# Kernel optimization log

Hardware: AMD Instinct MI355X
Metric: run time of the kernel (lower is better)

## Reference

```python
import jax, jax.numpy as jnp
import numpy as np
from jax import lax

GRID_SIZE = 5
SPLINE_ORDER = 3
N_COEF = GRID_SIZE + SPLINE_ORDER  # 8 b-spline basis functions per input
GRID_LO, GRID_HI = -1.0, 1.0


def _grid():
    h = (GRID_HI - GRID_LO) / GRID_SIZE
    return jnp.arange(-SPLINE_ORDER, GRID_SIZE + SPLINE_ORDER + 1, dtype=jnp.float32) * h + GRID_LO


def _bsplines(x):
    # x: [..., in] -> [..., in, N_COEF] via Cox-de Boor recursion (efficient-kan)
    grid = _grid()
    x = x[..., None]
    bases = ((x >= grid[:-1]) & (x < grid[1:])).astype(x.dtype)
    for j in range(1, SPLINE_ORDER + 1):
        bases = ((x - grid[:-(j + 1)]) / (grid[j:-1] - grid[:-(j + 1)]) * bases[..., :-1]
                 + (grid[j + 1:] - x) / (grid[j + 1:] - grid[1:-j]) * bases[..., 1:])
    return bases


def _kan_linear(x, base_w, spline_w):
    # x: [..., in]; base_w: [out, in]; spline_w: [out, in, N_COEF]
    base = jax.nn.silu(x) @ base_w.T
    b = _bsplines(x).reshape(x.shape[:-1] + (-1,))  # [..., in*N_COEF]
    return base + b @ spline_w.reshape(spline_w.shape[0], -1).T


def _kan_conv(x, base_w, spline_w):
    # x: [B, C, H, W]; 3x3 valid KAN convolution
    patches = lax.conv_general_dilated_patches(x, (3, 3), (1, 1), 'VALID')  # [B, C*9, H-2, W-2]
    p = patches.transpose(0, 2, 3, 1)  # [B, Ho, Wo, C*9]
    out = _kan_linear(p, base_w, spline_w)  # [B, Ho, Wo, out]
    return out.transpose(0, 3, 1, 2)


def _maxpool2(x):
    return lax.reduce_window(x, -jnp.inf, lax.max, (1, 1, 2, 2), (1, 1, 2, 2), 'VALID')


def setup_inputs() -> dict:
    key = jax.random.key(0)
    ks = jax.random.split(key, 12)
    B = 2048
    x = jax.random.uniform(ks[0], (B, 1, 28, 28), dtype=jnp.float32)
    s = 0.1
    return {
        'x': x,
        'bw1': jax.random.normal(ks[1], (5, 9), dtype=jnp.float32) * s,
        'sw1': jax.random.normal(ks[2], (5, 9, N_COEF), dtype=jnp.float32) * s,
        'bw2': jax.random.normal(ks[3], (5, 45), dtype=jnp.float32) * s,
        'sw2': jax.random.normal(ks[4], (5, 45, N_COEF), dtype=jnp.float32) * s,
        'bw3': jax.random.normal(ks[5], (2, 45), dtype=jnp.float32) * s,
        'sw3': jax.random.normal(ks[6], (2, 45, N_COEF), dtype=jnp.float32) * s,
        'w1': jax.random.normal(ks[7], (500, 162), dtype=jnp.float32) * 0.05,
        'b1': jnp.zeros((500,), dtype=jnp.float32),
        'w2': jax.random.normal(ks[8], (10, 500), dtype=jnp.float32) * 0.05,
        'b2': jnp.zeros((10,), dtype=jnp.float32),
    }


def reference(x, bw1, sw1, bw2, sw2, bw3, sw3, w1, b1, w2, b2):
    h = _kan_conv(x, bw1, sw1)       # [B, 5, 26, 26]
    h = _maxpool2(h)                 # [B, 5, 13, 13]
    h = _kan_conv(h, bw2, sw2)       # [B, 5, 11, 11]
    h = _kan_conv(h, bw3, sw3)       # [B, 2, 9, 9]
    h = h.reshape(h.shape[0], -1)    # [B, 162]
    h = jax.nn.relu(h @ w1.T + b1)   # [B, 500]
    return h @ w2.T + b2             # [B, 10]
```

## Files before the change

kernel.cpp:

```cpp
#include <hip/hip_runtime.h>


typedef _Float16 h2 __attribute__((ext_vector_type(2)));

__device__ __forceinline__ h2 u2h(unsigned int u) {
  union { unsigned int x; h2 h; } v; v.x = u; return v.h;
}
__device__ __forceinline__ unsigned short f2h_bits(float x) {
  union { _Float16 h; unsigned short u; } v; v.h = (_Float16)x; return v.u;
}
__device__ __forceinline__ float h2f(unsigned short u) {
  union { unsigned short u; _Float16 h; } v; v.u = u; return (float)v.h;
}
__device__ __forceinline__ unsigned int pack2h(float a, float b) {
  return (unsigned int)f2h_bits(a) | ((unsigned int)f2h_bits(b) << 16);
}
__device__ __forceinline__ float fdot2(h2 a, h2 b, float c) {
  return __builtin_amdgcn_fdot2(a, b, c, false);
}

__device__ __forceinline__ void featurize_regs(float v, uint4& bs, float& silu) {
  silu = v / (1.0f + __expf(-v));
  bs.x = 0u; bs.y = 0u; bs.z = 0u; bs.w = 0u;
  float u = fmaf(v, 2.5f, 5.5f);
  if (u >= 0.0f && u < 11.0f) {
    float tf = floorf(u);
    float f = u - tf, f2 = f * f, f3 = f2 * f, om = 1.0f - f;
    const float c6 = 1.0f / 6.0f;
    float w0 = om * om * om * c6;
    float w1 = (3.0f * f3 - 6.0f * f2 + 4.0f) * c6;
    float w2 = (-3.0f * f3 + 3.0f * f2 + 3.0f * f + 1.0f) * c6;
    float w3 = f3 * c6;
    unsigned long long w01 =
        (unsigned long long)f2h_bits(w0) |
        ((unsigned long long)f2h_bits(w1) << 16) |
        ((unsigned long long)f2h_bits(w2) << 32) |
        ((unsigned long long)f2h_bits(w3) << 48);
    int t = (int)tf;
    int s = 16 * t - 48;
    unsigned long long lo, hi;
    if (s >= 0) {
      lo = (s < 64) ? (w01 << s) : 0ull;
      hi = (s == 0) ? 0ull : ((s < 64) ? (w01 >> (64 - s)) : (w01 << (s - 64)));
    } else {
      lo = w01 >> (-s);
      hi = 0ull;
    }
    bs.x = (unsigned int)lo; bs.y = (unsigned int)(lo >> 32);
    bs.z = (unsigned int)hi; bs.w = (unsigned int)(hi >> 32);
  }
}

template <int NO, int CHS, int ROWW>
__device__ __forceinline__ void kconv_plain(
    const uint4* bas, const unsigned short* slu,
    const uint4* __restrict__ wS, const float* __restrict__ wB,
    int y0, int x0, float (&acc)[NO]) {
  const uint4* wp = wS;
  const float* bp = wB;
  int baC = y0 * ROWW + x0;
  #pragma unroll 1
  for (int c = 0; c < 5; ++c) {
    int ba = baC;
    #pragma unroll 1
    for (int ky = 0; ky < 3; ++ky) {
      uint4 q0 = bas[ba], q1 = bas[ba + 1], q2 = bas[ba + 2];
      float s0 = h2f(slu[ba]), s1 = h2f(slu[ba + 1]), s2 = h2f(slu[ba + 2]);
      #pragma unroll
      for (int kx = 0; kx < 3; ++kx) {
        uint4 q = (kx == 0) ? q0 : ((kx == 1) ? q1 : q2);
        float sl = (kx == 0) ? s0 : ((kx == 1) ? s1 : s2);
        h2 a0 = u2h(q.x), a1 = u2h(q.y), a2 = u2h(q.z), a3 = u2h(q.w);
        #pragma unroll
        for (int j = 0; j < NO; ++j) {
          uint4 w = wp[kx * NO + j];
          float a = acc[j];
          a = fdot2(a0, u2h(w.x), a);
          a = fdot2(a1, u2h(w.y), a);
          a = fdot2(a2, u2h(w.z), a);
          a = fdot2(a3, u2h(w.w), a);
          acc[j] = fmaf(sl, bp[kx * NO + j], a);
        }
      }
      wp += 3 * NO; bp += 3 * NO;
      ba += ROWW;
    }
    baC += CHS;
  }
}

__global__ __launch_bounds__(256) void k_prep(
    const float* __restrict__ bw1, const float* __restrict__ sw1,
    const float* __restrict__ bw2, const float* __restrict__ sw2,
    const float* __restrict__ bw3, const float* __restrict__ sw3,
    const float* __restrict__ w1, const float* __restrict__ w2,
    unsigned int* __restrict__ V1s, float* __restrict__ V1b,
    unsigned int* __restrict__ V2G0s, float* __restrict__ V2G0b,
    unsigned int* __restrict__ V2G1s, float* __restrict__ V2G1b,
    unsigned int* __restrict__ V3Gs, float* __restrict__ V3Gb,
    unsigned int* __restrict__ W1p4, float* __restrict__ W2p) {
  int t = blockIdx.x * 256 + threadIdx.x;
  if (t < 180) {
    int p = t & 3, o = (t >> 2) % 5, in = t / 20;
    V1s[t] = pack2h(sw1[(o * 9 + in) * 8 + 2 * p], sw1[(o * 9 + in) * 8 + 2 * p + 1]);
  }
  if (t < 45)  { int o = t % 5, in = t / 5; V1b[t] = bw1[o * 9 + in]; }
  if (t < 540) {
    int p = t & 3, u4 = t >> 2;
    int j = u4 % 3, kx = (u4 / 3) % 3, cky = u4 / 9;
    int in = (cky / 3) * 9 + (cky % 3) * 3 + kx;
    V2G0s[t] = pack2h(sw2[(j * 45 + in) * 8 + 2 * p], sw2[(j * 45 + in) * 8 + 2 * p + 1]);
  }
  if (t < 135) {
    int j = t % 3, kx = (t / 3) % 3, cky = t / 9;
    int in = (cky / 3) * 9 + (cky % 3) * 3 + kx;
    V2G0b[t] = bw2[j * 45 + in];
  }
  if (t < 360) {
    int p = t & 3, u4 = t >> 2;
    int j = u4 % 2, kx = (u4 / 2) % 3, cky = u4 / 6;
    int o = 3 + j;
    int in = (cky / 3) * 9 + (cky % 3) * 3 + kx;
    V2G1s[t] = pack2h(sw2[(o * 45 + in) * 8 + 2 * p], sw2[(o * 45 + in) * 8 + 2 * p + 1]);
  }
  if (t < 90) {
    int j = t % 2, kx = (t / 2) % 3, cky = t / 6;
    int o = 3 + j;
    int in = (cky / 3) * 9 + (cky % 3) * 3 + kx;
    V2G1b[t] = bw2[o * 45 + in];
  }
  if (t < 360) {
    int p = t & 3, u4 = t >> 2;
    int kx = u4 % 3, cky = (u4 / 3) % 15, ou = u4 / 45;
    int in = (cky / 3) * 9 + (cky % 3) * 3 + kx;
    V3Gs[t] = pack2h(sw3[(ou * 45 + in) * 8 + 2 * p], sw3[(ou * 45 + in) * 8 + 2 * p + 1]);
  }
  if (t < 90) {
    int kx = t % 3, cky = (t / 3) % 15, ou = t / 45;
    int in = (cky / 3) * 9 + (cky % 3) * 3 + kx;
    V3Gb[t] = bw3[ou * 45 + in];
  }
  if (t < 43008) {
    int j = t & 3, o = (t >> 2) & 511, g = t >> 11;
    int kp = g * 4 + j;
    W1p4[t] = (o < 500 && kp < 81)
                  ? pack2h(w1[o * 162 + 2 * kp], w1[o * 162 + 2 * kp + 1])
                  : 0u;
  }
  if (t < 5120) {
    int o = t >> 9, k = t & 511;
    W2p[t] = (k < 500) ? w2[o * 500 + k] : 0.0f;
  }
}

__global__ __launch_bounds__(256, 8) void k_fused(
    const float* __restrict__ x,
    const unsigned int* __restrict__ V1s, const float* __restrict__ V1b,
    const unsigned int* __restrict__ V2G0s, const float* __restrict__ V2G0b,
    const unsigned int* __restrict__ V2G1s, const float* __restrict__ V2G1b,
    const unsigned int* __restrict__ V3Gs, const float* __restrict__ V3Gb,
    const unsigned int* __restrict__ W1p4, const float* __restrict__ W2p,
    const float* __restrict__ b1, const float* __restrict__ b2,
    float* __restrict__ out) {
  __shared__ uint4 bas[845];
  __shared__ unsigned short slu16[848];
  __shared__ float red[40];
  float*        basF = (float*)bas;
  float*        h3f  = basF + 2048;
  unsigned int* hpk  = (unsigned int*)basF + 2560;
  const int b = blockIdx.x;
  const int tid = threadIdx.x;

  #pragma unroll 1
  for (int l = tid; l < 784; l += 256) {
    uint4 bs; float sl;
    featurize_regs(x[b * 784 + l], bs, sl);
    bas[l] = bs; slu16[l] = f2h_bits(sl);
  }
  __syncthreads();

  float h1v[5];
  if (tid < 169) {
    int py = tid / 13, px = tid % 13;
    int rowbase = (py * 2) * 28 + px * 2;
    float wacc[4][5];
    #pragma unroll
    for (int wi = 0; wi < 4; ++wi)
      #pragma unroll
      for (int o = 0; o < 5; ++o) wacc[wi][o] = 0.0f;
    const unsigned int* wp = V1s;
    const float* bp = V1b;
    int ba = rowbase;
    #pragma unroll 1
    for (int ky = 0; ky < 3; ++ky) {
      #pragma unroll 1
      for (int kx = 0; kx < 3; ++kx) {
        uint4 q00 = bas[ba],      q01 = bas[ba + 1];
        uint4 q10 = bas[ba + 28], q11 = bas[ba + 29];
        float s00 = h2f(slu16[ba]),      s01 = h2f(slu16[ba + 1]);
        float s10 = h2f(slu16[ba + 28]), s11 = h2f(slu16[ba + 29]);
        #pragma unroll
        for (int dy = 0; dy < 2; ++dy) {
          #pragma unroll
          for (int dx = 0; dx < 2; ++dx) {
            uint4 q  = dy ? (dx ? q11 : q10) : (dx ? q01 : q00);
            float sl = dy ? (dx ? s11 : s10) : (dx ? s01 : s00);
            h2 a0 = u2h(q.x), a1 = u2h(q.y), a2 = u2h(q.z), a3 = u2h(q.w);
            #pragma unroll
            for (int o = 0; o < 5; ++o) {
              float a = wacc[dy * 2 + dx][o];
              a = fdot2(a0, u2h(wp[o * 4 + 0]), a);
              a = fdot2(a1, u2h(wp[o * 4 + 1]), a);
              a = fdot2(a2, u2h(wp[o * 4 + 2]), a);
              a = fdot2(a3, u2h(wp[o * 4 + 3]), a);
              wacc[dy * 2 + dx][o] = fmaf(sl, bp[o], a);
            }
          }
        }
        wp += 20; bp += 5;
        ba += 1;
      }
      ba += 25;
    }
    #pragma unroll
    for (int o = 0; o < 5; ++o)
      h1v[o] = fmaxf(fmaxf(wacc[0][o], wacc[1][o]),
                     fmaxf(wacc[2][o], wacc[3][o]));
  }
  __syncthreads();
  if (tid < 169) {
    #pragma unroll
    for (int o = 0; o < 5; ++o) {
      uint4 bs; float sl;
      featurize_regs(h1v[o], bs, sl);
      bas[o * 169 + tid] = bs; slu16[o * 169 + tid] = f2h_bits(sl);
    }
  }
  __syncthreads();

  int og = __builtin_amdgcn_readfirstlane(tid >> 7);
  int p2 = tid & 127;
  float acc2a[3] = {0.0f, 0.0f, 0.0f};
  float acc2b[2] = {0.0f, 0.0f};
  {
    int pc = (p2 < 121) ? p2 : 120;
    int y0 = pc / 11, x0 = pc % 11;
    if (og == 0)
      kconv_plain<3, 169, 13>(bas, slu16, (const uint4*)V2G0s, V2G0b, y0, x0, acc2a);
    else
      kconv_plain<2, 169, 13>(bas, slu16, (const uint4*)V2G1s, V2G1b, y0, x0, acc2b);
  }
  __syncthreads();
  if (p2 < 121) {
    if (og == 0) {
      #pragma unroll
      for (int j = 0; j < 3; ++j) {
        uint4 bs; float sl;
        featurize_regs(acc2a[j], bs, sl);
        bas[j * 121 + p2] = bs; slu16[j * 121 + p2] = f2h_bits(sl);
      }
    } else {
      #pragma unroll
      for (int j = 0; j < 2; ++j) {
        uint4 bs; float sl;
        featurize_regs(acc2b[j], bs, sl);
        bas[(3 + j) * 121 + p2] = bs; slu16[(3 + j) * 121 + p2] = f2h_bits(sl);
      }
    }
  }
  __syncthreads();

  float acc3[1] = {0.0f};
  {
    int pc = (p2 < 81) ? p2 : 80;
    int y0 = pc / 9, x0 = pc % 9;
    kconv_plain<1, 121, 11>(bas, slu16, (const uint4*)V3Gs + og * 45,
                            V3Gb + og * 45, y0, x0, acc3);
  }
  __syncthreads();
  if (p2 < 81) h3f[og * 81 + p2] = acc3[0];
  __syncthreads();
  if (tid < 84)
    hpk[tid] = (tid < 81) ? pack2h(h3f[2 * tid], h3f[2 * tid + 1]) : 0u;
  __syncthreads();

  float fa[2] = {0.0f, 0.0f};
  {
    const uint4* hp4 = (const uint4*)hpk;
    const uint4* wbase = (const uint4*)W1p4 + tid;
    uint4 wA[2], wB[2];
    #pragma unroll
    for (int i = 0; i < 2; ++i) wA[i] = wbase[i * 256];
    #pragma unroll 1
    for (int g = 0; g < 21; g += 2) {
      if (g + 1 < 21) {
        const uint4* p = wbase + (g + 1) * 512;
        #pragma unroll
        for (int i = 0; i < 2; ++i) wB[i] = p[i * 256];
      }
      {
        uint4 hk = hp4[g];
        #pragma unroll
        for (int i = 0; i < 2; ++i) {
          float a = fa[i];
          a = fdot2(u2h(hk.x), u2h(wA[i].x), a);
          a = fdot2(u2h(hk.y), u2h(wA[i].y), a);
          a = fdot2(u2h(hk.z), u2h(wA[i].z), a);
          a = fdot2(u2h(hk.w), u2h(wA[i].w), a);
          fa[i] = a;
        }
      }
      if (g + 2 < 21) {
        const uint4* p = wbase + (g + 2) * 512;
        #pragma unroll
        for (int i = 0; i < 2; ++i) wA[i] = p[i * 256];
      }
      if (g + 1 < 21) {
        uint4 hk = hp4[g + 1];
        #pragma unroll
        for (int i = 0; i < 2; ++i) {
          float a = fa[i];
          a = fdot2(u2h(hk.x), u2h(wB[i].x), a);
          a = fdot2(u2h(hk.y), u2h(wB[i].y), a);
          a = fdot2(u2h(hk.z), u2h(wB[i].z), a);
          a = fdot2(u2h(hk.w), u2h(wB[i].w), a);
          fa[i] = a;
        }
      }
    }
  }
  #pragma unroll
  for (int i = 0; i < 2; ++i) {
    int o = tid + 256 * i;
    float bb = (o < 500) ? b1[o] : 0.0f;
    float v = fa[i] + bb;
    basF[o] = (v > 0.0f && o < 500) ? v : 0.0f;
  }
  __syncthreads();

  float acc10[10];
  {
    float2 ha = ((const float2*)basF)[tid];
    #pragma unroll
    for (int o = 0; o < 10; ++o) {
      float2 w = ((const float2*)&W2p[o * 512])[tid];
      acc10[o] = ha.x * w.x + ha.y * w.y;
    }
  }
  #pragma unroll
  for (int off = 32; off > 0; off >>= 1) {
    #pragma unroll
    for (int o = 0; o < 10; ++o) acc10[o] += __shfl_down(acc10[o], off);
  }
  if ((tid & 63) == 0) {
    int wid = tid >> 6;
    #pragma unroll
    for (int o = 0; o < 10; ++o) red[wid * 10 + o] = acc10[o];
  }
  __syncthreads();
  if (tid < 10)
    out[b * 10 + tid] = red[tid] + red[10 + tid] + red[20 + tid] + red[30 + tid] + b2[tid];
}

extern "C" void kernel_launch(void* const* d_in, const int* in_sizes, int n_in,
                              void* d_out, int out_size, void* d_ws, size_t ws_size,
                              hipStream_t stream) {
  (void)in_sizes; (void)n_in; (void)out_size; (void)ws_size;
  const float* x   = (const float*)d_in[0];
  const float* bw1 = (const float*)d_in[1];
  const float* sw1 = (const float*)d_in[2];
  const float* bw2 = (const float*)d_in[3];
  const float* sw2 = (const float*)d_in[4];
  const float* bw3 = (const float*)d_in[5];
  const float* sw3 = (const float*)d_in[6];
  const float* w1  = (const float*)d_in[7];
  const float* b1  = (const float*)d_in[8];
  const float* w2  = (const float*)d_in[9];
  const float* b2  = (const float*)d_in[10];
  float* out = (float*)d_out;

  char* ws = (char*)d_ws;
  unsigned int* V1s   = (unsigned int*)(ws);
  float*        V1b   = (float*)(ws + 768);
  unsigned int* V2G0s = (unsigned int*)(ws + 1024);
  unsigned int* V2G1s = (unsigned int*)(ws + 3200);
  unsigned int* V3Gs  = (unsigned int*)(ws + 4640);
  float*        V2G0b = (float*)(ws + 6080);
  float*        V2G1b = (float*)(ws + 6624);
  float*        V3Gb  = (float*)(ws + 6984);
  float*        W2p   = (float*)(ws + 7680);
  unsigned int* W1p4  = (unsigned int*)(ws + 28672);

  k_prep<<<168, 256, 0, stream>>>(bw1, sw1, bw2, sw2, bw3, sw3, w1, w2,
                                  V1s, V1b, V2G0s, V2G0b, V2G1s, V2G1b,
                                  V3Gs, V3Gb, W1p4, W2p);
  k_fused<<<2048, 256, 0, stream>>>(x, V1s, V1b, V2G0s, V2G0b, V2G1s, V2G1b,
                                    V3Gs, V3Gb, W1p4, W2p, b1, b2, out);
}
```

Measured before the change: 128.2 us.

## Move KAN conv layers 1 and 2 onto MFMA 16x16x32 f16 matrix ops

```diff
diff --git a/kernel.cpp b/kernel.cpp
--- a/kernel.cpp
+++ b/kernel.cpp
@@ -2,6 +2,10 @@
 
 
 typedef _Float16 h2 __attribute__((ext_vector_type(2)));
+typedef _Float16 f16x8 __attribute__((ext_vector_type(8)));
+typedef float f32x4 __attribute__((ext_vector_type(4)));
+
+union U4H { uint4 u; f16x8 h; };
 
 __device__ __forceinline__ h2 u2h(unsigned int u) {
   union { unsigned int x; h2 h; } v; v.x = u; return v.h;
@@ -17,6 +21,13 @@
 }
 __device__ __forceinline__ float fdot2(h2 a, h2 b, float c) {
   return __builtin_amdgcn_fdot2(a, b, c, false);
+}
+
+__device__ __forceinline__ constexpr int off1(int t) {
+  return (t / 3) * 28 + (t % 3);
+}
+__device__ __forceinline__ constexpr int off2v(int t) {
+  return (t / 9) * 169 + ((t % 9) / 3) * 13 + ((t % 9) % 3);
 }
 
 __device__ __forceinline__ void featurize_regs(float v, uint4& bs, float& silu) {
@@ -94,40 +105,43 @@
     const float* __restrict__ bw2, const float* __restrict__ sw2,
     const float* __restrict__ bw3, const float* __restrict__ sw3,
     const float* __restrict__ w1, const float* __restrict__ w2,
-    unsigned int* __restrict__ V1s, float* __restrict__ V1b,
-    unsigned int* __restrict__ V2G0s, float* __restrict__ V2G0b,
-    unsigned int* __restrict__ V2G1s, float* __restrict__ V2G1b,
+    unsigned int* __restrict__ Bc1g, unsigned int* __restrict__ B2g,
     unsigned int* __restrict__ V3Gs, float* __restrict__ V3Gb,
     unsigned int* __restrict__ W1p4, float* __restrict__ W2p) {
   int t = blockIdx.x * 256 + threadIdx.x;
-  if (t < 180) {
-    int p = t & 3, o = (t >> 2) % 5, in = t / 20;
-    V1s[t] = pack2h(sw1[(o * 9 + in) * 8 + 2 * p], sw1[(o * 9 + in) * 8 + 2 * p + 1]);
-  }
-  if (t < 45)  { int o = t % 5, in = t / 5; V1b[t] = bw1[o * 9 + in]; }
-  if (t < 540) {
-    int p = t & 3, u4 = t >> 2;
-    int j = u4 % 3, kx = (u4 / 3) % 3, cky = u4 / 9;
-    int in = (cky / 3) * 9 + (cky % 3) * 3 + kx;
-    V2G0s[t] = pack2h(sw2[(j * 45 + in) * 8 + 2 * p], sw2[(j * 45 + in) * 8 + 2 * p + 1]);
-  }
-  if (t < 135) {
-    int j = t % 3, kx = (t / 3) % 3, cky = t / 9;
-    int in = (cky / 3) * 9 + (cky % 3) * 3 + kx;
-    V2G0b[t] = bw2[j * 45 + in];
-  }
-  if (t < 360) {
-    int p = t & 3, u4 = t >> 2;
-    int j = u4 % 2, kx = (u4 / 2) % 3, cky = u4 / 6;
-    int o = 3 + j;
-    int in = (cky / 3) * 9 + (cky % 3) * 3 + kx;
-    V2G1s[t] = pack2h(sw2[(o * 45 + in) * 8 + 2 * p], sw2[(o * 45 + in) * 8 + 2 * p + 1]);
-  }
-  if (t < 90) {
-    int j = t % 2, kx = (t / 2) % 3, cky = t / 6;
-    int o = 3 + j;
-    int in = (cky / 3) * 9 + (cky % 3) * 3 + kx;
-    V2G1b[t] = bw2[o * 45 + in];
+  if (t < 1280) {
+    int i = t & 3, l = (t >> 2) & 63, s = t >> 8;
+    int k = s * 32 + ((l >> 4) & 3) * 8 + 2 * i;
+    int col = l & 15, tap = k >> 4, slot = k & 15;
+    unsigned int v = 0u;
+    if (col < 5 && tap < 9) {
+      if (slot < 8) {
+        const float* sp = sw1 + (col * 9 + tap) * 8 + slot;
+        v = pack2h(sp[0], sp[1]);
+      } else if (slot == 8) {
+        float bv = bw1[col * 9 + tap];
+        float hi = (float)(_Float16)bv;
+        v = pack2h(hi, bv - hi);
+      }
+    }
+    Bc1g[t] = v;
+  }
+  if (t < 5888) {
+    int i = t & 3, l = (t >> 2) & 63, s = t >> 8;
+    int k = s * 32 + ((l >> 4) & 3) * 8 + 2 * i;
+    int col = l & 15, tap = k >> 4, slot = k & 15;
+    unsigned int v = 0u;
+    if (col < 5 && tap < 45) {
+      if (slot < 8) {
+        const float* sp = sw2 + (col * 45 + tap) * 8 + slot;
+        v = pack2h(sp[0], sp[1]);
+      } else if (slot == 8) {
+        float bv = bw2[col * 45 + tap];
+        float hi = (float)(_Float16)bv;
+        v = pack2h(hi, bv - hi);
+      }
+    }
+    B2g[t] = v;
   }
   if (t < 360) {
     int p = t & 3, u4 = t >> 2;
@@ -153,140 +167,174 @@
   }
 }
 
-__global__ __launch_bounds__(256, 8) void k_fused(
+__global__ __launch_bounds__(256, 6) void k_fused(
     const float* __restrict__ x,
-    const unsigned int* __restrict__ V1s, const float* __restrict__ V1b,
-    const unsigned int* __restrict__ V2G0s, const float* __restrict__ V2G0b,
-    const unsigned int* __restrict__ V2G1s, const float* __restrict__ V2G1b,
+    const unsigned int* __restrict__ Bc1g, const unsigned int* __restrict__ B2g,
     const unsigned int* __restrict__ V3Gs, const float* __restrict__ V3Gb,
     const unsigned int* __restrict__ W1p4, const float* __restrict__ W2p,
     const float* __restrict__ b1, const float* __restrict__ b2,
     float* __restrict__ out) {
-  __shared__ uint4 bas[845];
-  __shared__ unsigned short slu16[848];
-  __shared__ float red[40];
-  float*        basF = (float*)bas;
-  float*        h3f  = basF + 2048;
-  unsigned int* hpk  = (unsigned int*)basF + 2560;
-  const int b = blockIdx.x;
+  __shared__ __attribute__((aligned(16))) char pool[23680];
+  uint4*          RECB = (uint4*)pool;
+  unsigned int*   INSP = (unsigned int*)(pool + 12544);
+  uint4*          H1B  = (uint4*)pool;
+  unsigned int*   H1SP = (unsigned int*)(pool + 13520);
+  unsigned short* WRES = (unsigned short*)(pool + 16900);
+  float*          C2   = (float*)(pool + 16900);
+  uint4*          H2B  = (uint4*)pool;
+  unsigned short* SLU2 = (unsigned short*)(pool + 9680);
+  float*          H3F  = (float*)(pool + 16900);
+  unsigned int*   HPK  = (unsigned int*)(pool + 17552);
+  float*          RED  = (float*)(pool + 17888);
+  unsigned int*   ZERO = (unsigned int*)(pool + 23664);
+  float*          BASF = (float*)pool;
+
+  const int b   = blockIdx.x;
   const int tid = threadIdx.x;
-
+  const int lane = tid & 63;
+  const int wv   = tid >> 6;
+  const int col  = lane & 15;
+  const int hi4  = lane >> 4;
+  const int haf  = hi4 & 1;
+  const int par  = hi4 >> 1;
+
+  if (tid < 4) ZERO[tid] = 0u;
   #pragma unroll 1
   for (int l = tid; l < 784; l += 256) {
     uint4 bs; float sl;
     featurize_regs(x[b * 784 + l], bs, sl);
-    bas[l] = bs; slu16[l] = f2h_bits(sl);
-  }
-  __syncthreads();
-
-  float h1v[5];
+    RECB[l] = bs; INSP[l] = pack2h(sl, sl);
+  }
+  __syncthreads();
+
+  {
+    U4H B1[5];
+    #pragma unroll
+    for (int s = 0; s < 5; ++s)
+      B1[s].u = ((const uint4*)Bc1g)[s * 64 + lane];
+    int mt0 = wv * 11;
+    int mtn = (wv < 3) ? 11 : 10;
+    #pragma unroll 1
+    for (int m = 0; m < mtn; ++m) {
+      int mt = mt0 + m;
+      int w = mt * 16 + col;
+      int wc = (w < 676) ? w : 675;
+      int wy = wc / 26;
+      int wbase = wy * 28 + (wc - wy * 26);
+      f32x4 acc = {0.f, 0.f, 0.f, 0.f};
+      #pragma unroll
+      for (int s = 0; s < 5; ++s) {
+        const int toV = 2 * s + 1;
+        int roff = par ? ((toV < 9) ? off1(toV) : 0) : off1(2 * s);
+        bool valid = (!par) || (toV < 9);
+        U4H a;
+        if (haf == 0) {
+          const uint4* ap = valid ? (RECB + (wbase + roff)) : (const uint4*)ZERO;
+          a.u = *ap;
+        } else {
+          const unsigned int* sp = valid ? (INSP + (wbase + roff)) : ZERO;
+          a.u.x = *sp; a.u.y = 0u; a.u.z = 0u; a.u.w = 0u;
+        }
+        acc = __builtin_amdgcn_mfma_f32_16x16x32_f16(a.h, B1[s].h, acc, 0, 0, 0);
+      }
+      if (col < 5) {
+        #pragma unroll
+        for (int r = 0; r < 4; ++r) {
+          int wr = mt * 16 + hi4 * 4 + r;
+          if (wr < 676) WRES[col * 676 + wr] = f2h_bits(acc[r]);
+        }
+      }
+    }
+  }
+  __syncthreads();
+
   if (tid < 169) {
-    int py = tid / 13, px = tid % 13;
-    int rowbase = (py * 2) * 28 + px * 2;
-    float wacc[4][5];
-    #pragma unroll
-    for (int wi = 0; wi < 4; ++wi)
+    int py = tid / 13, px = tid - (tid / 13) * 13;
+    int w00 = py * 52 + px * 2;
+    const unsigned int* W32 = (const unsigned int*)WRES;
+    #pragma unroll
+    for (int o = 0; o < 5; ++o) {
+      unsigned int a = W32[(o * 676 + w00) >> 1];
+      unsigned int c = W32[(o * 676 + w00 + 26) >> 1];
+      float v = fmaxf(fmaxf(h2f((unsigned short)a), h2f((unsigned short)(a >> 16))),
+                      fmaxf(h2f((unsigned short)c), h2f((unsigned short)(c >> 16))));
+      uint4 bs; float sl;
+      featurize_regs(v, bs, sl);
+      H1B[o * 169 + tid] = bs;
+      H1SP[o * 169 + tid] = pack2h(sl, sl);
+    }
+  }
+  __syncthreads();
+
+  {
+    int p0 = (wv * 2) * 16 + col;
+    int p1 = (wv * 2 + 1) * 16 + col;
+    int pc0 = (p0 < 121) ? p0 : 120;
+    int pc1 = (p1 < 121) ? p1 : 120;
+    int y0 = pc0 / 11, pb0 = y0 * 13 + (pc0 - y0 * 11);
+    int y1 = pc1 / 11, pb1 = y1 * 13 + (pc1 - y1 * 11);
+    f32x4 ac0 = {0.f, 0.f, 0.f, 0.f}, ac1 = {0.f, 0.f, 0.f, 0.f};
+    #pragma unroll
+    for (int s = 0; s < 23; ++s) {
+      const int toV = 2 * s + 1;
+      int roff = par ? ((toV < 45) ? off2v(toV) : 0) : off2v(2 * s);
+      bool valid = (!par) || (toV < 45);
+      U4H bf; bf.u = ((const uint4*)B2g)[s * 64 + lane];
+      U4H a0, a1;
+      if (haf == 0) {
+        const uint4* q0 = valid ? (H1B + (pb0 + roff)) : (const uint4*)ZERO;
+        const uint4* q1 = valid ? (H1B + (pb1 + roff)) : (const uint4*)ZERO;
+        a0.u = *q0; a1.u = *q1;
+      } else {
+        const unsigned int* s0p = valid ? (H1SP + (pb0 + roff)) : ZERO;
+        const unsigned int* s1p = valid ? (H1SP + (pb1 + roff)) : ZERO;
+        a0.u.x = *s0p; a0.u.y = 0u; a0.u.z = 0u; a0.u.w = 0u;
+        a1.u.x = *s1p; a1.u.y = 0u; a1.u.z = 0u; a1.u.w = 0u;
+      }
+      ac0 = __builtin_amdgcn_mfma_f32_16x16x32_f16(a0.h, bf.h, ac0, 0, 0, 0);
+      ac1 = __builtin_amdgcn_mfma_f32_16x16x32_f16(a1.h, bf.h, ac1, 0, 0, 0);
+    }
+    if (col < 5) {
       #pragma unroll
-      for (int o = 0; o < 5; ++o) wacc[wi][o] = 0.0f;
-    const unsigned int* wp = V1s;
-    const float* bp = V1b;
-    int ba = rowbase;
-    #pragma unroll 1
-    for (int ky = 0; ky < 3; ++ky) {
-      #pragma unroll 1
-      for (int kx = 0; kx < 3; ++kx) {
-        uint4 q00 = bas[ba],      q01 = bas[ba + 1];
-        uint4 q10 = bas[ba + 28], q11 = bas[ba + 29];
-        float s00 = h2f(slu16[ba]),      s01 = h2f(slu16[ba + 1]);
-        float s10 = h2f(slu16[ba + 28]), s11 = h2f(slu16[ba + 29]);
-        #pragma unroll
-        for (int dy = 0; dy < 2; ++dy) {
-          #pragma unroll
-          for (int dx = 0; dx < 2; ++dx) {
-            uint4 q  = dy ? (dx ? q11 : q10) : (dx ? q01 : q00);
-            float sl = dy ? (dx ? s11 : s10) : (dx ? s01 : s00);
-            h2 a0 = u2h(q.x), a1 = u2h(q.y), a2 = u2h(q.z), a3 = u2h(q.w);
-            #pragma unroll
-            for (int o = 0; o < 5; ++o) {
-              float a = wacc[dy * 2 + dx][o];
-              a = fdot2(a0, u2h(wp[o * 4 + 0]), a);
-              a = fdot2(a1, u2h(wp[o * 4 + 1]), a);
-              a = fdot2(a2, u2h(wp[o * 4 + 2]), a);
-              a = fdot2(a3, u2h(wp[o * 4 + 3]), a);
-              wacc[dy * 2 + dx][o] = fmaf(sl, bp[o], a);
-            }
-          }
-        }
-        wp += 20; bp += 5;
-        ba += 1;
-      }
-      ba += 25;
-    }
-    #pragma unroll
-    for (int o = 0; o < 5; ++o)
-      h1v[o] = fmaxf(fmaxf(wacc[0][o], wacc[1][o]),
-                     fmaxf(wacc[2][o], wacc[3][o]));
-  }
-  __syncthreads();
-  if (tid < 169) {
-    #pragma unroll
-    for (int o = 0; o < 5; ++o) {
+      for (int r = 0; r < 4; ++r) {
+        C2[col * 128 + (wv * 2) * 16 + hi4 * 4 + r]     = ac0[r];
+        C2[col * 128 + (wv * 2 + 1) * 16 + hi4 * 4 + r] = ac1[r];
+      }
+    }
+  }
+  __syncthreads();
+
+  #pragma unroll 1
+  for (int k2 = 0; k2 < 3; ++k2) {
+    int it = tid + 256 * k2;
+    if (it < 605) {
+      int o = it / 121, p = it - o * 121;
       uint4 bs; float sl;
-      featurize_regs(h1v[o], bs, sl);
-      bas[o * 169 + tid] = bs; slu16[o * 169 + tid] = f2h_bits(sl);
+      featurize_regs(C2[o * 128 + p], bs, sl);
+      H2B[o * 121 + p] = bs;
+      SLU2[o * 121 + p] = f2h_bits(sl);
     }
   }
   __syncthreads();
 
   int og = __builtin_amdgcn_readfirstlane(tid >> 7);
   int p2 = tid & 127;
-  float acc2a[3] = {0.0f, 0.0f, 0.0f};
-  float acc2b[2] = {0.0f, 0.0f};
-  {
-    int pc = (p2 < 121) ? p2 : 120;
-    int y0 = pc / 11, x0 = pc % 11;
-    if (og == 0)
-      kconv_plain<3, 169, 13>(bas, slu16, (const uint4*)V2G0s, V2G0b, y0, x0, acc2a);
-    else
-      kconv_plain<2, 169, 13>(bas, slu16, (const uint4*)V2G1s, V2G1b, y0, x0, acc2b);
-  }
-  __syncthreads();
-  if (p2 < 121) {
-    if (og == 0) {
-      #pragma unroll
-      for (int j = 0; j < 3; ++j) {
-        uint4 bs; float sl;
-        featurize_regs(acc2a[j], bs, sl);
-        bas[j * 121 + p2] = bs; slu16[j * 121 + p2] = f2h_bits(sl);
-      }
-    } else {
-      #pragma unroll
-      for (int j = 0; j < 2; ++j) {
-        uint4 bs; float sl;
-        featurize_regs(acc2b[j], bs, sl);
-        bas[(3 + j) * 121 + p2] = bs; slu16[(3 + j) * 121 + p2] = f2h_bits(sl);
-      }
-    }
-  }
-  __syncthreads();
-
   float acc3[1] = {0.0f};
   {
     int pc = (p2 < 81) ? p2 : 80;
-    int y0 = pc / 9, x0 = pc % 9;
-    kconv_plain<1, 121, 11>(bas, slu16, (const uint4*)V3Gs + og * 45,
+    int y0 = pc / 9, x0 = pc - (pc / 9) * 9;
+    kconv_plain<1, 121, 11>(H2B, SLU2, (const uint4*)V3Gs + og * 45,
                             V3Gb + og * 45, y0, x0, acc3);
   }
-  __syncthreads();
-  if (p2 < 81) h3f[og * 81 + p2] = acc3[0];
+  if (p2 < 81) H3F[og * 81 + p2] = acc3[0];
   __syncthreads();
   if (tid < 84)
-    hpk[tid] = (tid < 81) ? pack2h(h3f[2 * tid], h3f[2 * tid + 1]) : 0u;
+    HPK[tid] = (tid < 81) ? pack2h(H3F[2 * tid], H3F[2 * tid + 1]) : 0u;
   __syncthreads();
 
   float fa[2] = {0.0f, 0.0f};
   {
-    const uint4* hp4 = (const uint4*)hpk;
+    const uint4* hp4 = (const uint4*)HPK;
     const uint4* wbase = (const uint4*)W1p4 + tid;
     uint4 wA[2], wB[2];
     #pragma unroll
@@ -334,13 +382,13 @@
     int o = tid + 256 * i;
     float bb = (o < 500) ? b1[o] : 0.0f;
     float v = fa[i] + bb;
-    basF[o] = (v > 0.0f && o < 500) ? v : 0.0f;
+    BASF[o] = (v > 0.0f && o < 500) ? v : 0.0f;
   }
   __syncthreads();
 
   float acc10[10];
   {
-    float2 ha = ((const float2*)basF)[tid];
+    float2 ha = ((const float2*)BASF)[tid];
     #pragma unroll
     for (int o = 0; o < 10; ++o) {
       float2 w = ((const float2*)&W2p[o * 512])[tid];
@@ -355,11 +403,11 @@
   if ((tid & 63) == 0) {
     int wid = tid >> 6;
     #pragma unroll
-    for (int o = 0; o < 10; ++o) red[wid * 10 + o] = acc10[o];
+    for (int o = 0; o < 10; ++o) RED[wid * 10 + o] = acc10[o];
   }
   __syncthreads();
   if (tid < 10)
-    out[b * 10 + tid] = red[tid] + red[10 + tid] + red[20 + tid] + red[30 + tid] + b2[tid];
+    out[b * 10 + tid] = RED[tid] + RED[10 + tid] + RED[20 + tid] + RED[30 + tid] + b2[tid];
 }
 
 extern "C" void kernel_launch(void* const* d_in, const int* in_sizes, int n_in,
@@ -380,20 +428,15 @@
   float* out = (float*)d_out;
 
   char* ws = (char*)d_ws;
-  unsigned int* V1s   = (unsigned int*)(ws);
-  float*        V1b   = (float*)(ws + 768);
-  unsigned int* V2G0s = (unsigned int*)(ws + 1024);
-  unsigned int* V2G1s = (unsigned int*)(ws + 3200);
-  unsigned int* V3Gs  = (unsigned int*)(ws + 4640);
-  float*        V2G0b = (float*)(ws + 6080);
-  float*        V2G1b = (float*)(ws + 6624);
-  float*        V3Gb  = (float*)(ws + 6984);
-  float*        W2p   = (float*)(ws + 7680);
-  unsigned int* W1p4  = (unsigned int*)(ws + 28672);
+  unsigned int* Bc1g = (unsigned int*)(ws);
+  unsigned int* B2g  = (unsigned int*)(ws + 5120);
+  unsigned int* V3Gs = (unsigned int*)(ws + 28672);
+  float*        V3Gb = (float*)(ws + 30112);
+  float*        W2p  = (float*)(ws + 30720);
+  unsigned int* W1p4 = (unsigned int*)(ws + 51200);
 
   k_prep<<<168, 256, 0, stream>>>(bw1, sw1, bw2, sw2, bw3, sw3, w1, w2,
-                                  V1s, V1b, V2G0s, V2G0b, V2G1s, V2G1b,
-                                  V3Gs, V3Gb, W1p4, W2p);
-  k_fused<<<2048, 256, 0, stream>>>(x, V1s, V1b, V2G0s, V2G0b, V2G1s, V2G1b,
-                                    V3Gs, V3Gb, W1p4, W2p, b1, b2, out);
-}
+                                  Bc1g, B2g, V3Gs, V3Gb, W1p4, W2p);
+  k_fused<<<2048, 256, 0, stream>>>(x, Bc1g, B2g, V3Gs, V3Gb,
+                                    W1p4, W2p, b1, b2, out);
+}
```

Result: no change. 130.5 us (+1.8%).
